# Kernel tuning notes

Hardware: AMD Instinct MI355X
Metric: run time of the kernel (lower is better)

The kernel has to match this reference:

```python
import jax, jax.numpy as jnp
import numpy as np

B, S, D, H_FF, E, NH, K = 8, 1024, 128, 512, 4, 8, 2


def setup_inputs() -> dict:
    key = jax.random.key(0)
    ks = jax.random.split(key, 8)
    g = lambda k, shape, s=0.02: jax.random.normal(k, shape, dtype=jnp.float32) * s
    return {
        "x": jax.random.normal(ks[0], (B, S, D), dtype=jnp.float32),
        "Wqkv": g(ks[1], (D, 3 * D)),
        "bqkv": jnp.zeros((3 * D,), jnp.float32),
        "Wo": g(ks[2], (D, D)),
        "bo": jnp.zeros((D,), jnp.float32),
        "n1_w": jnp.ones((D,), jnp.float32),
        "n1_b": jnp.zeros((D,), jnp.float32),
        "n2_w": jnp.ones((D,), jnp.float32),
        "n2_b": jnp.zeros((D,), jnp.float32),
        "w_gate": g(ks[3], (D, E)),
        "W1": g(ks[4], (E, D, H_FF)),
        "b1": jnp.zeros((E, H_FF), jnp.float32),
        "W2": g(ks[5], (E, H_FF, D)),
        "b2": jnp.zeros((E, D), jnp.float32),
        "num_heads": NH,
        "topk": K,
    }


def _instance_norm(x, w, b, eps=1e-5):
    # InstanceNorm1d applied over the sequence axis, per (batch, channel), affine per channel
    mu = x.mean(axis=1, keepdims=True)
    var = x.var(axis=1, keepdims=True)  # biased variance, as in torch InstanceNorm
    return (x - mu) * jax.lax.rsqrt(var + eps) * w + b


def _cv_sq(v, eps=1e-10):
    return v.var(ddof=1) / (v.mean() ** 2 + eps)


def _forward(x, Wqkv, bqkv, Wo, bo, n1_w, n1_b, n2_w, n2_b, w_gate, W1, b1, W2, b2, num_heads, topk):
    B_, S_, D_ = x.shape
    hd = D_ // num_heads
    # --- MHA ---
    qkv = x @ Wqkv + bqkv  # [B,S,3D]
    q, k, v = jnp.split(qkv, 3, axis=-1)
    rs = lambda t: t.reshape(B_, S_, num_heads, hd).transpose(0, 2, 1, 3)  # [B,H,S,hd]
    q, k, v = rs(q), rs(k), rs(v)
    scores = jnp.einsum('bhqd,bhkd->bhqk', q, k) / jnp.sqrt(jnp.float32(hd))
    attn = jax.nn.softmax(scores, axis=-1)
    o = jnp.einsum('bhqk,bhkd->bhqd', attn, v).transpose(0, 2, 1, 3).reshape(B_, S_, D_)
    h = _instance_norm(o @ Wo + bo + x, n1_w, n1_b)
    # --- MoE feedforward: node-level top-k gating (eval mode: no gating noise) ---
    flat = h.reshape(-1, D_)                      # [N, D], N = B*S tokens
    logits = flat @ w_gate                        # [N, E]
    top_logits, top_idx = jax.lax.top_k(logits, topk)
    top_gates = jax.nn.softmax(top_logits, axis=-1)
    N = flat.shape[0]
    gates = jnp.zeros_like(logits).at[jnp.arange(N)[:, None], top_idx].set(top_gates)
    hid = jax.nn.relu(jnp.einsum('nd,edh->neh', flat, W1) + b1)   # [N,E,H]
    eo = jnp.einsum('neh,ehd->ned', hid, W2) + b2                 # [N,E,D]
    y = jnp.einsum('ne,ned->nd', gates, eo).reshape(B_, S_, D_)
    importance = gates.sum(axis=0)
    load = (gates > 0).astype(jnp.float32).sum(axis=0)
    moe_loss = _cv_sq(importance) + _cv_sq(load)
    out = _instance_norm(y + h, n2_w, n2_b)
    return out, moe_loss


def reference(x, Wqkv, bqkv, Wo, bo, n1_w, n1_b, n2_w, n2_b, w_gate, W1, b1, W2, b2, num_heads, topk):
    out, _moe_loss = _forward(x, Wqkv, bqkv, Wo, bo, n1_w, n1_b, n2_w, n2_b,
                              w_gate, W1, b1, W2, b2, num_heads, topk)
    return out
```

## Files before the change

kernel.cpp:

```cpp
#include <hip/hip_runtime.h>
#include <hip/hip_bf16.h>

#define B_   8
#define S_   1024
#define D_   128
#define NH_  8
#define HD_  16
#define E_   4
#define HFF_ 512
#define NTOK (B_*S_)

typedef unsigned short ushort_t;
typedef __attribute__((ext_vector_type(8))) short bf16x8;
typedef __attribute__((ext_vector_type(4))) float f32x4;
typedef __attribute__((ext_vector_type(4))) _Float16 f16x4;

static __device__ __forceinline__ ushort_t f2bf(float f) {
    union { float f; unsigned u; } v; v.f = f;
    unsigned r = v.u + 0x7FFF + ((v.u >> 16) & 1);
    return (ushort_t)(r >> 16);
}
static __device__ __forceinline__ float bf2f(ushort_t u) {
    union { unsigned u; float f; } v; v.u = ((unsigned)u) << 16;
    return v.f;
}

__global__ __launch_bounds__(256)
void prep(const float* __restrict__ Wqkv, const float* __restrict__ Wo,
          const float* __restrict__ W1, const float* __restrict__ W2,
          ushort_t* __restrict__ Wqkv_t, ushort_t* __restrict__ Wo_t,
          ushort_t* __restrict__ W1t, ushort_t* __restrict__ W2t)
{
    const int seg = blockIdx.y;
    const int i = blockIdx.x * 256 + threadIdx.x;
    if (seg == 0) {
        if (i < D_ * 3 * D_) {
            int r = i / (3 * D_), c = i % (3 * D_);
            Wqkv_t[c * D_ + r] = f2bf(Wqkv[i]);
        }
    } else if (seg == 1) {
        if (i < D_ * D_) {
            int r = i >> 7, c = i & 127;
            Wo_t[c * D_ + r] = f2bf(Wo[i]);
        }
    } else if (seg == 2) {
        int e = i >> 16, rem = i & 65535, r = rem >> 9, c = rem & 511;
        W1t[e * 65536 + c * 128 + r] = f2bf(W1[i]);
    } else {
        int e = i >> 16, rem = i & 65535, k2 = rem >> 7, dd = rem & 127;
        W2t[e * 65536 + dd * 512 + k2] = f2bf(W2[i]);
    }
}

__global__ __launch_bounds__(256)
void gemm_qkv(const float* __restrict__ x, const ushort_t* __restrict__ Bt,
              const float* __restrict__ bias,
              _Float16* __restrict__ pq, _Float16* __restrict__ pk,
              _Float16* __restrict__ pv)
{
    __shared__ __align__(16) ushort_t As[4][128][8];
    __shared__ __align__(16) ushort_t Bs[4][128][8];
    const int bm = blockIdx.x * 128;
    const int bn = blockIdx.y * 128;
    const int part = blockIdx.y;
    const int tid = threadIdx.x;
    const int l = tid & 63, wv = tid >> 6;
    const int lc = l & 15, lg = l >> 4;
    const int wr = wv >> 1, wc = wv & 1;
    const int K = D_;

    f32x4 acc[4][4] = {};

    const int srow = tid & 127, sch = tid >> 7;
    const float*    ap = x  + (size_t)(bm + srow) * K + sch * 8;
    const ushort_t* bp = Bt + (size_t)(bn + srow) * K + sch * 8;

    for (int k0 = 0; k0 < K; k0 += 32) {
        #pragma unroll
        for (int half = 0; half < 2; half++) {
            float4 v0 = *(const float4*)(ap + k0 + half * 16);
            float4 v1 = *(const float4*)(ap + k0 + half * 16 + 4);
            bf16x8 pk8;
            pk8[0] = (short)f2bf(v0.x); pk8[1] = (short)f2bf(v0.y);
            pk8[2] = (short)f2bf(v0.z); pk8[3] = (short)f2bf(v0.w);
            pk8[4] = (short)f2bf(v1.x); pk8[5] = (short)f2bf(v1.y);
            pk8[6] = (short)f2bf(v1.z); pk8[7] = (short)f2bf(v1.w);
            *(bf16x8*)As[sch + half * 2][srow] = pk8;
        }
        *(bf16x8*)Bs[sch][srow]     = *(const bf16x8*)(bp + k0);
        *(bf16x8*)Bs[sch + 2][srow] = *(const bf16x8*)(bp + k0 + 16);
        __syncthreads();
        bf16x8 af[4], bfr[4];
        #pragma unroll
        for (int f = 0; f < 4; f++) {
            af[f]  = *(const bf16x8*)As[lg][wr * 64 + f * 16 + lc];
            bfr[f] = *(const bf16x8*)Bs[lg][wc * 64 + f * 16 + lc];
        }
        #pragma unroll
        for (int fm = 0; fm < 4; fm++)
            #pragma unroll
            for (int fn = 0; fn < 4; fn++)
                acc[fm][fn] = __builtin_amdgcn_mfma_f32_16x16x32_bf16(
                    af[fm], bfr[fn], acc[fm][fn], 0, 0, 0);
        __syncthreads();
    }

    #pragma unroll
    for (int fm = 0; fm < 4; fm++) {
        #pragma unroll
        for (int fn = 0; fn < 4; fn++) {
            const int col = bn + wc * 64 + fn * 16 + lc;
            const int hh = (col >> 4) & 7, dd = col & 15;
            const int row0 = bm + wr * 64 + fm * 16 + lg * 4;
            const int b = row0 >> 10, s0 = row0 & 1023;
            const size_t bh = (size_t)(b * NH_ + hh);
            const float bcol = bias[col];
            if (part == 2) {
                f16x4 vv;
                #pragma unroll
                for (int rr = 0; rr < 4; rr++)
                    vv[rr] = (_Float16)(acc[fm][fn][rr] + bcol);
                *(f16x4*)&pv[(bh << 14) + (dd << 10) + s0] = vv;
            } else {
                const float sc = (part == 0) ? 0.36067376022224085f : 1.f;
                _Float16* dst = (part == 0) ? pq : pk;
                #pragma unroll
                for (int rr = 0; rr < 4; rr++)
                    dst[(bh * 1024 + s0 + rr) * HD_ + dd] =
                        (_Float16)((acc[fm][fn][rr] + bcol) * sc);
            }
        }
    }
}

__global__ __launch_bounds__(256)
void gemm_out(const ushort_t* __restrict__ attno, const ushort_t* __restrict__ Wo_t,
              const float* __restrict__ bo, const float* __restrict__ x,
              float* __restrict__ t, float* __restrict__ pstatA)
{
    __shared__ __align__(16) ushort_t As[4][64][8];
    __shared__ __align__(16) ushort_t Bs[4][128][8];
    __shared__ float2 sred[4][128];
    const int tok0 = blockIdx.x * 64;
    const int tid = threadIdx.x;
    const int l = tid & 63, wv = tid >> 6;
    const int lc = l & 15, lg = l >> 4;

    f32x4 acc[8] = {};

    const int arow = tid & 63, akc = tid >> 6;
    const int bn = tid & 127, bj = tid >> 7;
    const ushort_t* ap = attno + (size_t)(tok0 + arow) * D_ + akc * 8;
    const ushort_t* bp = Wo_t + (size_t)bn * D_ + bj * 16;

    for (int k0 = 0; k0 < 128; k0 += 32) {
        *(bf16x8*)As[akc][arow]     = *(const bf16x8*)(ap + k0);
        *(bf16x8*)Bs[bj * 2][bn]     = *(const bf16x8*)(bp + k0);
        *(bf16x8*)Bs[bj * 2 + 1][bn] = *(const bf16x8*)(bp + k0 + 8);
        __syncthreads();
        bf16x8 af = *(const bf16x8*)As[lg][wv * 16 + lc];
        #pragma unroll
        for (int fn = 0; fn < 8; fn++) {
            bf16x8 bf = *(const bf16x8*)Bs[lg][fn * 16 + lc];
            acc[fn] = __builtin_amdgcn_mfma_f32_16x16x32_bf16(af, bf, acc[fn], 0, 0, 0);
        }
        __syncthreads();
    }

    const int bb = tok0 >> 10, c16 = (tok0 >> 6) & 15;
    #pragma unroll
    for (int fn = 0; fn < 8; fn++) {
        const int col = fn * 16 + lc;
        float s = 0.f, q = 0.f;
        #pragma unroll
        for (int rr = 0; rr < 4; rr++) {
            const int row = wv * 16 + lg * 4 + rr;
            const size_t off = (size_t)(tok0 + row) * D_ + col;
            float v = acc[fn][rr] + bo[col] + x[off];
            t[off] = v;
            s += v; q += v * v;
        }
        s += __shfl_xor(s, 16); q += __shfl_xor(q, 16);
        s += __shfl_xor(s, 32); q += __shfl_xor(q, 32);
        if (l < 16) sred[wv][col] = make_float2(s, q);
    }
    __syncthreads();
    if (tid < 128) {
        float2 a0 = sred[0][tid], a1 = sred[1][tid], a2 = sred[2][tid], a3 = sred[3][tid];
        ((float2*)pstatA)[(bb * 16 + c16) * D_ + tid] =
            make_float2(a0.x + a1.x + a2.x + a3.x, a0.y + a1.y + a2.y + a3.y);
    }
}

__global__ __launch_bounds__(256)
void moe_fused(const float* __restrict__ t, const float* __restrict__ pstatA,
               const float* __restrict__ n1w, const float* __restrict__ n1b,
               const float* __restrict__ wg,
               const ushort_t* __restrict__ W1t, const ushort_t* __restrict__ W2t,
               const float* __restrict__ b1, const float* __restrict__ b2,
               ushort_t* __restrict__ ypartb)
{
    __shared__ __align__(16) ushort_t As[16][64][8];
    __shared__ __align__(16) ushort_t HS[16][64][8];
    __shared__ float2 sst[128];
    __shared__ float4 glog[4][64];
    __shared__ float garr[64];
    const int tok0 = blockIdx.x * 64, e = blockIdx.y;
    const int tid = threadIdx.x;
    const int l = tid & 63, wv = tid >> 6;
    const int lc = l & 15, lg = l >> 4;
    const int bb = tok0 >> 10;

    if (tid < 128) {
        float sum = 0.f, sq = 0.f;
        const float2* pp = (const float2*)pstatA;
        #pragma unroll 4
        for (int c = 0; c < 16; c++) {
            float2 v = pp[(bb * 16 + c) * D_ + tid];
            sum += v.x; sq += v.y;
        }
        const float invS = 1.f / (float)S_;
        float mu = sum * invS;
        float var = sq * invS - mu * mu;
        sst[tid] = make_float2(mu, rsqrtf(var + 1e-5f));
    }
    __syncthreads();

    {
        const int row = tid & 63, part = tid >> 6;
        const float* src = t + (size_t)(tok0 + row) * D_ + part * 32;
        float4 aa = make_float4(0.f, 0.f, 0.f, 0.f);
        #pragma unroll
        for (int j = 0; j < 4; j++) {
            bf16x8 pk8;
            #pragma unroll
            for (int half = 0; half < 2; half++) {
                float4 v = *(const float4*)(src + j * 8 + half * 4);
                const int db = part * 32 + j * 8 + half * 4;
                float hv[4] = {v.x, v.y, v.z, v.w};
                #pragma unroll
                for (int c = 0; c < 4; c++) {
                    float2 s = sst[db + c];
                    hv[c] = (hv[c] - s.x) * s.y * n1w[db + c] + n1b[db + c];
                    float4 wj = ((const float4*)wg)[db + c];
                    aa.x += hv[c] * wj.x; aa.y += hv[c] * wj.y;
                    aa.z += hv[c] * wj.z; aa.w += hv[c] * wj.w;
                    pk8[half * 4 + c] = (short)f2bf(hv[c]);
                }
            }
            *(bf16x8*)As[part * 4 + j][row] = pk8;
        }
        glog[part][row] = aa;
    }
    __syncthreads();
    if (tid < 64) {
        float4 a0 = glog[0][tid], a1 = glog[1][tid], a2 = glog[2][tid], a3 = glog[3][tid];
        float lv[4] = {a0.x + a1.x + a2.x + a3.x, a0.y + a1.y + a2.y + a3.y,
                       a0.z + a1.z + a2.z + a3.z, a0.w + a1.w + a2.w + a3.w};
        int i0 = 0; float mm0 = lv[0];
        #pragma unroll
        for (int k = 1; k < 4; k++) if (lv[k] > mm0) { mm0 = lv[k]; i0 = k; }
        int i1 = -1; float mm1 = -1e30f;
        #pragma unroll
        for (int k = 0; k < 4; k++) {
            if (k == i0) continue;
            if (lv[k] > mm1) { mm1 = lv[k]; i1 = k; }
        }
        float te = __expf(mm1 - mm0);
        float g0 = 1.f / (1.f + te);
        float g1 = te * g0;
        garr[tid] = (e == i0) ? g0 : (e == i1) ? g1 : 0.f;
    }
    __syncthreads();

    const ushort_t* W1e = W1t + (size_t)e * HFF_ * D_;
    const ushort_t* W2e = W2t + (size_t)e * D_ * HFF_;
    const int col0 = wv * 32 + lc;

    f32x4 acc2[4][2] = {};

    #pragma unroll 1
    for (int c = 0; c < 4; c++) {
        bf16x8 w1f[4][2], w2f[4][2];
        #pragma unroll
        for (int ks = 0; ks < 4; ks++)
            #pragma unroll
            for (int fn = 0; fn < 2; fn++) {
                w1f[ks][fn] = *(const bf16x8*)&W1e[(size_t)(c * 128 + col0 + fn * 16) * D_ + ks * 32 + lg * 8];
                w2f[ks][fn] = *(const bf16x8*)&W2e[(size_t)(col0 + fn * 16) * HFF_ + c * 128 + ks * 32 + lg * 8];
            }
        f32x4 acc1[4][2] = {};
        #pragma unroll
        for (int ks = 0; ks < 4; ks++) {
            bf16x8 af[4];
            #pragma unroll
            for (int f = 0; f < 4; f++) af[f] = *(const bf16x8*)As[ks * 4 + lg][f * 16 + lc];
            #pragma unroll
            for (int fm = 0; fm < 4; fm++)
                #pragma unroll
                for (int fn = 0; fn < 2; fn++)
                    acc1[fm][fn] = __builtin_amdgcn_mfma_f32_16x16x32_bf16(
                        af[fm], w1f[ks][fn], acc1[fm][fn], 0, 0, 0);
        }
        __syncthreads();
        #pragma unroll
        for (int fm = 0; fm < 4; fm++)
            #pragma unroll
            for (int fn = 0; fn < 2; fn++)
                #pragma unroll
                for (int rr = 0; rr < 4; rr++) {
                    const int row = fm * 16 + lg * 4 + rr;
                    const int col = wv * 32 + fn * 16 + lc;
                    float v = fmaxf(acc1[fm][fn][rr] + b1[e * HFF_ + c * 128 + col], 0.f);
                    HS[col >> 3][row][col & 7] = f2bf(v);
                }
        __syncthreads();
        #pragma unroll
        for (int ks2 = 0; ks2 < 4; ks2++) {
            bf16x8 af[4];
            #pragma unroll
            for (int f = 0; f < 4; f++) af[f] = *(const bf16x8*)HS[ks2 * 4 + lg][f * 16 + lc];
            #pragma unroll
            for (int fm = 0; fm < 4; fm++)
                #pragma unroll
                for (int fn = 0; fn < 2; fn++)
                    acc2[fm][fn] = __builtin_amdgcn_mfma_f32_16x16x32_bf16(
                        af[fm], w2f[ks2][fn], acc2[fm][fn], 0, 0, 0);
        }
    }

    #pragma unroll
    for (int fm = 0; fm < 4; fm++)
        #pragma unroll
        for (int rr = 0; rr < 4; rr++) {
            const int row = fm * 16 + lg * 4 + rr;
            const float g = garr[row];
            #pragma unroll
            for (int fn = 0; fn < 2; fn++) {
                const int d = wv * 32 + fn * 16 + lc;
                ypartb[((size_t)e * NTOK + tok0 + row) * D_ + d] =
                    f2bf(g * (acc2[fm][fn][rr] + b2[e * D_ + d]));
            }
        }
}

#define KT_STR 20
#define VT_STR 136

__global__ __launch_bounds__(512)
void attn_mfma(const _Float16* __restrict__ Qb, const _Float16* __restrict__ Kb,
               const _Float16* __restrict__ Vt, ushort_t* __restrict__ attno)
{
    __shared__ __align__(16) _Float16 KT[2][128 * KT_STR];
    __shared__ __align__(16) _Float16 VTs[2][16 * VT_STR];
    const int bh = blockIdx.x;
    const int tid = threadIdx.x;
    const int wv = tid >> 6;
    const int l  = tid & 63;
    const int r = l & 15, g = l >> 4;
    const int g4 = g * 4;
    const int q0 = blockIdx.y * 128 + wv * 16;

    const _Float16* qp = Qb + ((size_t)bh << 14);
    const _Float16* kp = Kb + ((size_t)bh << 14);
    const _Float16* vp = Vt + ((size_t)bh << 14);

    f16x4 qf = *(const f16x4*)&qp[(q0 + r) * HD_ + g4];

    const int krow = tid >> 2, kq = tid & 3;
    const int kofs = krow * KT_STR + kq * 4;
    const _Float16* kg = kp + krow * HD_ + kq * 4;
    const int vrow = tid >> 5, vsc = tid & 31;
    const int vofs = vrow * VT_STR + vsc * 4;
    const _Float16* vg = vp + vrow * 1024 + vsc * 4;

    const int kbase = r * KT_STR + g4;
    const int vbase = r * VT_STR + g4;

    f32x4 o = {};
    float lp = 0.f;

    {
        *(f16x4*)&KT[0][kofs]  = *(const f16x4*)kg;
        *(f16x4*)&VTs[0][vofs] = *(const f16x4*)vg;
    }
    __syncthreads();

    int cur = 0;
    #pragma unroll 1
    for (int t = 0; t < 8; t++) {
        f16x4 kr, vr;
        if (t < 7) {
            kr = *(const f16x4*)(kg + (t + 1) * 2048);
            vr = *(const f16x4*)(vg + (t + 1) * 128);
        }
        const _Float16* KTc = KT[cur];
        const _Float16* VTc = VTs[cur];
        #pragma unroll
        for (int kt = 0; kt < 8; kt++) {
            f16x4 kf = *(const f16x4*)&KTc[kbase + kt * (16 * KT_STR)];
            f16x4 vf = *(const f16x4*)&VTc[vbase + kt * 16];
            f32x4 z = {};
            f32x4 s0 = __builtin_amdgcn_mfma_f32_16x16x16f16(kf, qf, z, 0, 0, 0);
            float p0 = exp2f(s0[0]), p1 = exp2f(s0[1]), p2 = exp2f(s0[2]), p3 = exp2f(s0[3]);
            lp += (p0 + p1) + (p2 + p3);
            f16x4 pf;
            pf[0] = (_Float16)p0; pf[1] = (_Float16)p1;
            pf[2] = (_Float16)p2; pf[3] = (_Float16)p3;
            o = __builtin_amdgcn_mfma_f32_16x16x16f16(vf, pf, o, 0, 0, 0);
        }
        if (t < 7) {
            *(f16x4*)&KT[cur ^ 1][kofs]  = kr;
            *(f16x4*)&VTs[cur ^ 1][vofs] = vr;
        }
        __syncthreads();
        cur ^= 1;
    }

    lp += __shfl_xor(lp, 16);
    lp += __shfl_xor(lp, 32);
    const float inv = 1.f / lp;

    const int b = bh >> 3, h = bh & 7;
    ushort4 out;
    out.x = f2bf(o[0] * inv); out.y = f2bf(o[1] * inv);
    out.z = f2bf(o[2] * inv); out.w = f2bf(o[3] * inv);
    *(ushort4*)&attno[((size_t)(b * S_ + q0 + r)) * D_ + h * HD_ + g4] = out;
}

__global__ __launch_bounds__(128)
void moe_reduce_stats(const ushort_t* __restrict__ ypartb, const float* __restrict__ t,
                      const float* __restrict__ pstatA,
                      const float* __restrict__ n1w, const float* __restrict__ n1b,
                      ushort_t* __restrict__ yhb, float* __restrict__ pstatB)
{
    const int bb = blockIdx.x, chunk = blockIdx.y, d = threadIdx.x;

    float sum0 = 0.f, sq0 = 0.f;
    const float2* pp = (const float2*)pstatA;
    #pragma unroll 4
    for (int c = 0; c < 16; c++) {
        float2 v = pp[(bb * 16 + c) * D_ + d];
        sum0 += v.x; sq0 += v.y;
    }
    const float invS = 1.f / (float)S_;
    const float mu = sum0 * invS;
    const float rstd = rsqrtf(sq0 * invS - mu * mu + 1e-5f);
    const float wd = n1w[d], bd = n1b[d];

    float sum = 0.f, sq = 0.f;
    for (int s = 0; s < 32; s++) {
        const size_t off = ((size_t)bb * 1024 + chunk * 32 + s) * D_ + d;
        float hv = (t[off] - mu) * rstd * wd + bd;
        float v = hv
                + bf2f(ypartb[off])
                + bf2f(ypartb[(size_t)1 * NTOK * D_ + off])
                + bf2f(ypartb[(size_t)2 * NTOK * D_ + off])
                + bf2f(ypartb[(size_t)3 * NTOK * D_ + off]);
        yhb[off] = f2bf(v);
        sum += v; sq += v * v;
    }
    ((float2*)pstatB)[(bb * 32 + chunk) * D_ + d] = make_float2(sum, sq);
}

__global__ __launch_bounds__(256)
void in_apply_final(const ushort_t* __restrict__ a, const float* __restrict__ pstatB,
                    const float* __restrict__ w, const float* __restrict__ bias,
                    float* __restrict__ outp)
{
    __shared__ float2 sst[128];
    const int tid = threadIdx.x;
    const int bb = (int)((blockIdx.x * 8) >> 10);
    if (tid < 128) {
        float sum = 0.f, sq = 0.f;
        const float2* pp = (const float2*)pstatB;
        #pragma unroll 4
        for (int c = 0; c < 32; c++) {
            float2 v = pp[(bb * 32 + c) * D_ + tid];
            sum += v.x; sq += v.y;
        }
        const float invS = 1.f / (float)S_;
        float mu = sum * invS;
        float var = sq * invS - mu * mu;
        sst[tid] = make_float2(mu, rsqrtf(var + 1e-5f));
    }
    __syncthreads();

    size_t i4 = (size_t)blockIdx.x * 256 + tid;
    int d0 = (tid & 31) * 4;
    ushort4 u = ((const ushort4*)a)[i4];
    float4 v = make_float4(bf2f(u.x), bf2f(u.y), bf2f(u.z), bf2f(u.w));
    float2 s0 = sst[d0 + 0];
    float2 s1 = sst[d0 + 1];
    float2 s2 = sst[d0 + 2];
    float2 s3 = sst[d0 + 3];
    float4 r;
    r.x = (v.x - s0.x) * s0.y * w[d0 + 0] + bias[d0 + 0];
    r.y = (v.y - s1.x) * s1.y * w[d0 + 1] + bias[d0 + 1];
    r.z = (v.z - s2.x) * s2.y * w[d0 + 2] + bias[d0 + 2];
    r.w = (v.w - s3.x) * s3.y * w[d0 + 3] + bias[d0 + 3];
    ((float4*)outp)[i4] = r;
}

extern "C" void kernel_launch(void* const* d_in, const int* in_sizes, int n_in,
                              void* d_out, int out_size, void* d_ws, size_t ws_size,
                              hipStream_t stream)
{
    const float* x    = (const float*)d_in[0];
    const float* Wqkv = (const float*)d_in[1];
    const float* bqkv = (const float*)d_in[2];
    const float* Wo   = (const float*)d_in[3];
    const float* bo   = (const float*)d_in[4];
    const float* n1w  = (const float*)d_in[5];
    const float* n1b  = (const float*)d_in[6];
    const float* n2w  = (const float*)d_in[7];
    const float* n2b  = (const float*)d_in[8];
    const float* wg   = (const float*)d_in[9];
    const float* W1   = (const float*)d_in[10];
    const float* b1   = (const float*)d_in[11];
    const float* W2   = (const float*)d_in[12];
    const float* b2   = (const float*)d_in[13];

    char* ws = (char*)d_ws;
    _Float16* Qb     = (_Float16*)(ws);
    _Float16* Kb     = (_Float16*)(ws + (2u << 20));
    _Float16* Vt     = (_Float16*)(ws + (4u << 20));
    ushort_t* attno  = (ushort_t*)(ws + (6u << 20));
    float*    t      = (float*)(ws + (8u << 20));
    ushort_t* ypartb = (ushort_t*)(ws + (14u << 20));
    ushort_t* yhb    = (ushort_t*)(ws + (22u << 20));
    char*     wbase  = ws + (26u << 20);
    ushort_t* Wqkv_t = (ushort_t*)(wbase);
    ushort_t* Wo_t   = (ushort_t*)(wbase + (128u << 10));
    ushort_t* W1t    = (ushort_t*)(wbase + (192u << 10));
    ushort_t* W2t    = (ushort_t*)(wbase + (704u << 10));
    float*    pstatA = (float*)(wbase + (1216u << 10));
    float*    pstatB = (float*)(wbase + (1344u << 10));

    dim3 blk(256);

    prep<<<dim3(1024, 4), blk, 0, stream>>>(Wqkv, Wo, W1, W2,
                                            Wqkv_t, Wo_t, W1t, W2t);
    gemm_qkv<<<dim3(64, 3), blk, 0, stream>>>(x, Wqkv_t, bqkv, Qb, Kb, Vt);
    attn_mfma<<<dim3(64, 8), dim3(512), 0, stream>>>(Qb, Kb, Vt, attno);
    gemm_out<<<dim3(128), blk, 0, stream>>>(attno, Wo_t, bo, x, t, pstatA);
    moe_fused<<<dim3(128, 4), blk, 0, stream>>>(t, pstatA, n1w, n1b, wg,
                                                W1t, W2t, b1, b2, ypartb);
    moe_reduce_stats<<<dim3(B_, 32), dim3(128), 0, stream>>>(ypartb, t, pstatA,
                                                             n1w, n1b, yhb, pstatB);
    in_apply_final<<<dim3(1024), blk, 0, stream>>>(yhb, pstatB, n2w, n2b,
                                                   (float*)d_out);
}
```

Before: 91.74 us.

## Process two query tiles per wave in attention and fully unroll MoE chunk loop

Each attention wave now handles 32 query rows, as two 16-row MFMA tiles, instead of 16. Every K/V fragment loaded from LDS is reused twice, and the grid is halved to 64x4 blocks, so K/V staging traffic per query drops. The MoE fused kernel's chunk loop is also fully unrolled. Both changes raise register pressure, and the smaller attention grid (256 blocks) may leave compute units underused.

```diff
diff --git a/kernel.cpp b/kernel.cpp
--- a/kernel.cpp
+++ b/kernel.cpp
@@ -279,7 +279,7 @@
 
     f32x4 acc2[4][2] = {};
 
-    #pragma unroll 1
+    #pragma unroll
     for (int c = 0; c < 4; c++) {
         bf16x8 w1f[4][2], w2f[4][2];
         #pragma unroll
@@ -359,13 +359,14 @@
     const int l  = tid & 63;
     const int r = l & 15, g = l >> 4;
     const int g4 = g * 4;
-    const int q0 = blockIdx.y * 128 + wv * 16;
+    const int q0 = blockIdx.y * 256 + wv * 32;
 
     const _Float16* qp = Qb + ((size_t)bh << 14);
     const _Float16* kp = Kb + ((size_t)bh << 14);
     const _Float16* vp = Vt + ((size_t)bh << 14);
 
-    f16x4 qf = *(const f16x4*)&qp[(q0 + r) * HD_ + g4];
+    f16x4 qf0 = *(const f16x4*)&qp[(q0 + r) * HD_ + g4];
+    f16x4 qf1 = *(const f16x4*)&qp[(q0 + 16 + r) * HD_ + g4];
 
     const int krow = tid >> 2, kq = tid & 3;
     const int kofs = krow * KT_STR + kq * 4;
@@ -377,8 +378,8 @@
     const int kbase = r * KT_STR + g4;
     const int vbase = r * VT_STR + g4;
 
-    f32x4 o = {};
-    float lp = 0.f;
+    f32x4 o0 = {}, o1 = {};
+    float lp0 = 0.f, lp1 = 0.f;
 
     {
         *(f16x4*)&KT[0][kofs]  = *(const f16x4*)kg;
@@ -401,13 +402,19 @@
             f16x4 kf = *(const f16x4*)&KTc[kbase + kt * (16 * KT_STR)];
             f16x4 vf = *(const f16x4*)&VTc[vbase + kt * 16];
             f32x4 z = {};
-            f32x4 s0 = __builtin_amdgcn_mfma_f32_16x16x16f16(kf, qf, z, 0, 0, 0);
+            f32x4 s0 = __builtin_amdgcn_mfma_f32_16x16x16f16(kf, qf0, z, 0, 0, 0);
+            f32x4 s1 = __builtin_amdgcn_mfma_f32_16x16x16f16(kf, qf1, z, 0, 0, 0);
             float p0 = exp2f(s0[0]), p1 = exp2f(s0[1]), p2 = exp2f(s0[2]), p3 = exp2f(s0[3]);
-            lp += (p0 + p1) + (p2 + p3);
-            f16x4 pf;
-            pf[0] = (_Float16)p0; pf[1] = (_Float16)p1;
-            pf[2] = (_Float16)p2; pf[3] = (_Float16)p3;
-            o = __builtin_amdgcn_mfma_f32_16x16x16f16(vf, pf, o, 0, 0, 0);
+            float p4 = exp2f(s1[0]), p5 = exp2f(s1[1]), p6 = exp2f(s1[2]), p7 = exp2f(s1[3]);
+            lp0 += (p0 + p1) + (p2 + p3);
+            lp1 += (p4 + p5) + (p6 + p7);
+            f16x4 pf0, pf1;
+            pf0[0] = (_Float16)p0; pf0[1] = (_Float16)p1;
+            pf0[2] = (_Float16)p2; pf0[3] = (_Float16)p3;
+            pf1[0] = (_Float16)p4; pf1[1] = (_Float16)p5;
+            pf1[2] = (_Float16)p6; pf1[3] = (_Float16)p7;
+            o0 = __builtin_amdgcn_mfma_f32_16x16x16f16(vf, pf0, o0, 0, 0, 0);
+            o1 = __builtin_amdgcn_mfma_f32_16x16x16f16(vf, pf1, o1, 0, 0, 0);
         }
         if (t < 7) {
             *(f16x4*)&KT[cur ^ 1][kofs]  = kr;
@@ -417,15 +424,18 @@
         cur ^= 1;
     }
 
-    lp += __shfl_xor(lp, 16);
-    lp += __shfl_xor(lp, 32);
-    const float inv = 1.f / lp;
+    lp0 += __shfl_xor(lp0, 16); lp0 += __shfl_xor(lp0, 32);
+    lp1 += __shfl_xor(lp1, 16); lp1 += __shfl_xor(lp1, 32);
+    const float inv0 = 1.f / lp0, inv1 = 1.f / lp1;
 
     const int b = bh >> 3, h = bh & 7;
-    ushort4 out;
-    out.x = f2bf(o[0] * inv); out.y = f2bf(o[1] * inv);
-    out.z = f2bf(o[2] * inv); out.w = f2bf(o[3] * inv);
-    *(ushort4*)&attno[((size_t)(b * S_ + q0 + r)) * D_ + h * HD_ + g4] = out;
+    ushort4 out0, out1;
+    out0.x = f2bf(o0[0] * inv0); out0.y = f2bf(o0[1] * inv0);
+    out0.z = f2bf(o0[2] * inv0); out0.w = f2bf(o0[3] * inv0);
+    out1.x = f2bf(o1[0] * inv1); out1.y = f2bf(o1[1] * inv1);
+    out1.z = f2bf(o1[2] * inv1); out1.w = f2bf(o1[3] * inv1);
+    *(ushort4*)&attno[((size_t)(b * S_ + q0 + r)) * D_ + h * HD_ + g4] = out0;
+    *(ushort4*)&attno[((size_t)(b * S_ + q0 + 16 + r)) * D_ + h * HD_ + g4] = out1;
 }
 
 __global__ __launch_bounds__(128)
@@ -542,7 +552,7 @@
     prep<<<dim3(1024, 4), blk, 0, stream>>>(Wqkv, Wo, W1, W2,
                                             Wqkv_t, Wo_t, W1t, W2t);
     gemm_qkv<<<dim3(64, 3), blk, 0, stream>>>(x, Wqkv_t, bqkv, Qb, Kb, Vt);
-    attn_mfma<<<dim3(64, 8), dim3(512), 0, stream>>>(Qb, Kb, Vt, attno);
+    attn_mfma<<<dim3(64, 4), dim3(512), 0, stream>>>(Qb, Kb, Vt, attno);
     gemm_out<<<dim3(128), blk, 0, stream>>>(attno, Wo_t, bo, x, t, pstatA);
     moe_fused<<<dim3(128, 4), blk, 0, stream>>>(t, pstatA, n1w, n1b, wg,
                                                 W1t, W2t, b1, b2, ypartb);
```

After: 92.42 us. About the same (+0.7%).
